# Kernel tuning notes

Measured on AMD Instinct MI355X. Metric: run time of the kernel, lower is better.

## Reference

```python
import jax, jax.numpy as jnp
import numpy as np

N_NODES = 100000
N_EDGES = 600000
IN_FEATS = 128
N_HIDDEN = 128
N_CLASSES = 64


def _glorot(key, shape):
    fan_in, fan_out = shape[1], shape[0]
    lim = np.sqrt(6.0 / (fan_in + fan_out)).astype(np.float32)
    return jax.random.uniform(key, shape, jnp.float32, -lim, lim)


def setup_inputs() -> dict:
    key = jax.random.key(0)
    ks = jax.random.split(key, 12)
    x = jax.random.normal(ks[0], (N_NODES, IN_FEATS), jnp.float32)
    edge_src = jax.random.randint(ks[1], (N_EDGES,), 0, N_NODES, jnp.int64 if jax.config.jax_enable_x64 else jnp.int32)
    edge_dst = jax.random.randint(ks[2], (N_EDGES,), 0, N_NODES, jnp.int64 if jax.config.jax_enable_x64 else jnp.int32)
    dims = [(IN_FEATS, N_HIDDEN), (N_HIDDEN, N_HIDDEN), (N_HIDDEN, N_CLASSES)]
    inp = {"x": x, "edge_src": edge_src, "edge_dst": edge_dst}
    for i, (din, dout) in enumerate(dims, start=1):
        inp[f"W_self{i}"] = _glorot(ks[2 + 3 * i], (dout, din))
        inp[f"W_neigh{i}"] = _glorot(ks[3 + 3 * i], (dout, din))
        inp[f"b{i}"] = jnp.zeros((dout,), jnp.float32)
    return inp


def _sage_conv(h, edge_src, edge_dst, W_self, W_neigh, b):
    # mean-aggregate neighbor features: gather at src, segment-mean at dst
    msgs = h[edge_src]                                   # [E, din] irregular gather
    agg = jax.ops.segment_sum(msgs, edge_dst, num_segments=h.shape[0])
    deg = jax.ops.segment_sum(jnp.ones_like(edge_dst, dtype=h.dtype), edge_dst,
                              num_segments=h.shape[0])
    h_neigh = agg / jnp.maximum(deg, 1.0)[:, None]
    # fc_self(h) + fc_neigh(h_neigh) + bias  (DGL SAGEConv 'mean')
    return h @ W_self.T + h_neigh @ W_neigh.T + b


def reference(x, edge_src, edge_dst,
              W_self1, W_neigh1, b1,
              W_self2, W_neigh2, b2,
              W_self3, W_neigh3, b3):
    h = _sage_conv(x, edge_src, edge_dst, W_self1, W_neigh1, b1)
    h = jax.nn.relu(h)  # dropout is identity at inference
    h = _sage_conv(h, edge_src, edge_dst, W_self2, W_neigh2, b2)
    h = jax.nn.relu(h)
    h = _sage_conv(h, edge_src, edge_dst, W_self3, W_neigh3, b3)
    return h
```

## Files before the change

kernel.cpp:

```cpp
#include <hip/hip_runtime.h>

#define NN 100000
#define NE 600000
#define FD 128
#define NB ((NN + 255) / 256)

typedef __attribute__((ext_vector_type(8))) short bf16x8;
typedef __attribute__((ext_vector_type(4))) float f32x4;

__device__ __forceinline__ unsigned short f2bf(float x) {
    unsigned int u = __float_as_uint(x);
    u += 0x7FFFu + ((u >> 16) & 1u);
    return (unsigned short)(u >> 16);
}

__global__ __launch_bounds__(256) void hist_kernel(const int* __restrict__ dst,
                                                   int* __restrict__ cnt, int E) {
    int e = blockIdx.x * 256 + threadIdx.x;
    if (e < E) atomicAdd(&cnt[dst[e]], 1);
}

__global__ __launch_bounds__(256) void scan_blocks(const int* __restrict__ cnt,
                                                   int* __restrict__ bsum) {
    __shared__ int s[256];
    int i = blockIdx.x * 256 + threadIdx.x;
    int t = threadIdx.x;
    s[t] = (i < NN) ? cnt[i] : 0;
    __syncthreads();
    for (int off = 128; off > 0; off >>= 1) {
        if (t < off) s[t] += s[t + off];
        __syncthreads();
    }
    if (t == 0) bsum[blockIdx.x] = s[0];
}

__global__ __launch_bounds__(512) void scan_top(int* __restrict__ bsum,
                                                int* __restrict__ row_ptr) {
    __shared__ int s[512];
    int t = threadIdx.x;
    int v = (t < NB) ? bsum[t] : 0;
    s[t] = v;
    __syncthreads();
    for (int off = 1; off < 512; off <<= 1) {
        int x = (t >= off) ? s[t - off] : 0;
        __syncthreads();
        s[t] += x;
        __syncthreads();
    }
    if (t < NB) bsum[t] = s[t] - v;
    if (t == 0) row_ptr[NN] = NE;
}

__global__ __launch_bounds__(256) void scan_write(const int* __restrict__ cnt,
                                                  const int* __restrict__ bofs,
                                                  int* __restrict__ row_ptr) {
    __shared__ int s[256];
    int i = blockIdx.x * 256 + threadIdx.x;
    int t = threadIdx.x;
    int v = (i < NN) ? cnt[i] : 0;
    s[t] = v;
    __syncthreads();
    for (int off = 1; off < 256; off <<= 1) {
        int x = (t >= off) ? s[t - off] : 0;
        __syncthreads();
        s[t] += x;
        __syncthreads();
    }
    if (i < NN) row_ptr[i] = s[t] - v + bofs[blockIdx.x];
}

__global__ __launch_bounds__(256) void fill_kernel(const int* __restrict__ src,
                                                   const int* __restrict__ dst,
                                                   int* __restrict__ cursor,
                                                   int* __restrict__ col, int E) {
    int e = blockIdx.x * 256 + threadIdx.x;
    if (e < E) {
        int p = atomicAdd(&cursor[dst[e]], 1);
        col[p] = src[e];
    }
}

__global__ __launch_bounds__(256) void cvt_kernel(const float* __restrict__ x,
                                                  unsigned short* __restrict__ xb,
                                                  int n4) {
    int i = blockIdx.x * 256 + threadIdx.x;
    if (i < n4) {
        float4 v = reinterpret_cast<const float4*>(x)[i];
        uint2 o;
        o.x = (unsigned)f2bf(v.x) | ((unsigned)f2bf(v.y) << 16);
        o.y = (unsigned)f2bf(v.z) | ((unsigned)f2bf(v.w) << 16);
        reinterpret_cast<uint2*>(xb)[i] = o;
    }
}

__global__ __launch_bounds__(256) void wcvt_kernel(const float* __restrict__ Ws,
                                                   const float* __restrict__ Wn,
                                                   unsigned short* __restrict__ Wb,
                                                   int rows) {
    int tid = blockIdx.x * 256 + threadIdx.x;
    if (tid >= rows * 64) return;
    int row = tid >> 6;
    int k   = (tid & 63) * 4;
    const float* src = (k < 128) ? (Ws + (size_t)row * 128 + k)
                                 : (Wn + (size_t)row * 128 + (k - 128));
    float4 v = *reinterpret_cast<const float4*>(src);
    uint2 o;
    o.x = (unsigned)f2bf(v.x) | ((unsigned)f2bf(v.y) << 16);
    o.y = (unsigned)f2bf(v.z) | ((unsigned)f2bf(v.w) << 16);
    *reinterpret_cast<uint2*>(Wb + (size_t)row * 256 + k) = o;
}

__device__ __forceinline__ void bf2_acc(unsigned v, float& ax, float& ay) {
    ax += __uint_as_float(v << 16);
    ay += __uint_as_float(v & 0xFFFF0000u);
}

__global__ __launch_bounds__(256) void agg_kernel(const unsigned short* __restrict__ h,
                                                  const int* __restrict__ rp,
                                                  const int* __restrict__ col,
                                                  unsigned short* __restrict__ agg) {
    int w    = (blockIdx.x * 256 + threadIdx.x) >> 6;
    int lane = threadIdx.x & 63;
    if (w >= NN) return;
    int beg = __builtin_amdgcn_readfirstlane(rp[w]);
    int end = __builtin_amdgcn_readfirstlane(rp[w + 1]);
    const unsigned short* hl = h + lane * 2;
    float ax = 0.f, ay = 0.f;
    int e = beg;
    for (; e + 4 <= end; e += 4) {
        int s0 = col[e + 0], s1 = col[e + 1], s2 = col[e + 2], s3 = col[e + 3];
        unsigned v0 = *reinterpret_cast<const unsigned*>(hl + (size_t)s0 * FD);
        unsigned v1 = *reinterpret_cast<const unsigned*>(hl + (size_t)s1 * FD);
        unsigned v2 = *reinterpret_cast<const unsigned*>(hl + (size_t)s2 * FD);
        unsigned v3 = *reinterpret_cast<const unsigned*>(hl + (size_t)s3 * FD);
        bf2_acc(v0, ax, ay);
        bf2_acc(v1, ax, ay);
        bf2_acc(v2, ax, ay);
        bf2_acc(v3, ax, ay);
    }
    if (e + 2 <= end) {
        int s0 = col[e + 0], s1 = col[e + 1];
        unsigned v0 = *reinterpret_cast<const unsigned*>(hl + (size_t)s0 * FD);
        unsigned v1 = *reinterpret_cast<const unsigned*>(hl + (size_t)s1 * FD);
        bf2_acc(v0, ax, ay);
        bf2_acc(v1, ax, ay);
        e += 2;
    }
    if (e < end) {
        int s0 = col[e];
        unsigned v0 = *reinterpret_cast<const unsigned*>(hl + (size_t)s0 * FD);
        bf2_acc(v0, ax, ay);
    }
    float inv = 1.0f / fmaxf((float)(end - beg), 1.0f);
    ax *= inv;
    ay *= inv;
    *reinterpret_cast<unsigned*>(agg + (size_t)w * FD + lane * 2) =
        (unsigned)f2bf(ax) | ((unsigned)f2bf(ay) << 16);
}

template <int BN, bool RELU, bool OUTBF16>
__global__ __launch_bounds__(256, 3) void mfma_gemm(const unsigned short* __restrict__ Ah,
                                                    const unsigned short* __restrict__ Ag,
                                                    const unsigned short* __restrict__ Wb,
                                                    const float* __restrict__ bias,
                                                    void* __restrict__ outp, int N) {
    __shared__ char lds[16384 + BN * 256];
    char* Al = lds;
    char* Bl = lds + 16384;

    const int t   = threadIdx.x;
    const int n0  = blockIdx.x * 64;
    const int w   = t >> 6;
    const int l   = t & 63;
    const int lo4 = l & 15;
    const int hi  = l >> 4;
    const int xr  = (lo4 & 7) << 4;

    f32x4 acc[BN / 16];
#pragma unroll
    for (int f = 0; f < BN / 16; ++f) acc[f] = {0.f, 0.f, 0.f, 0.f};

#pragma unroll
    for (int kc = 0; kc < 2; ++kc) {
        const unsigned short* Asrc = kc ? Ag : Ah;
#pragma unroll
        for (int p = 0; p < 4; ++p) {
            int c   = t + p * 256;
            int row = c >> 4;
            int ch  = c & 15;
            int n   = n0 + row;
            uint4 v = make_uint4(0u, 0u, 0u, 0u);
            if (n < N) v = *reinterpret_cast<const uint4*>(Asrc + (size_t)n * FD + ch * 8);
            *reinterpret_cast<uint4*>(Al + ((row * 256 + ch * 16) ^ ((row & 7) << 4))) = v;
        }
#pragma unroll
        for (int p = 0; p < BN / 16; ++p) {
            int c   = t + p * 256;
            int row = c >> 4;
            int ch  = c & 15;
            uint4 v = *reinterpret_cast<const uint4*>(Wb + (size_t)row * 256 + kc * 128 + ch * 8);
            *reinterpret_cast<uint4*>(Bl + ((row * 256 + ch * 16) ^ ((row & 7) << 4))) = v;
        }
        __syncthreads();

        const char* Arow = Al + (w * 16 + lo4) * 256;
#pragma unroll
        for (int ks = 0; ks < 4; ++ks) {
            int koff = (ks * 64 + hi * 16) ^ xr;
            bf16x8 a = *reinterpret_cast<const bf16x8*>(Arow + koff);
#pragma unroll
            for (int f = 0; f < BN / 16; ++f) {
                bf16x8 b = *reinterpret_cast<const bf16x8*>(Bl + (f * 16 + lo4) * 256 + koff);
                acc[f] = __builtin_amdgcn_mfma_f32_16x16x32_bf16(a, b, acc[f], 0, 0, 0);
            }
        }
        __syncthreads();
    }

    unsigned short* hout = (unsigned short*)outp;
    float* fout = (float*)outp;
    const int rbase = n0 + w * 16 + hi * 4;
#pragma unroll
    for (int f = 0; f < BN / 16; ++f) {
        int col  = f * 16 + lo4;
        float bv = bias[col];
#pragma unroll
        for (int r = 0; r < 4; ++r) {
            int n = rbase + r;
            if (n < N) {
                float v = acc[f][r] + bv;
                if (RELU) v = fmaxf(v, 0.f);
                if (OUTBF16) hout[(size_t)n * 128 + col] = f2bf(v);
                else         fout[(size_t)n * BN + col] = v;
            }
        }
    }
}

extern "C" void kernel_launch(void* const* d_in, const int* in_sizes, int n_in,
                              void* d_out, int out_size, void* d_ws, size_t ws_size,
                              hipStream_t stream) {
    const float* x        = (const float*)d_in[0];
    const int*   edge_src = (const int*)d_in[1];
    const int*   edge_dst = (const int*)d_in[2];
    const float* Ws1 = (const float*)d_in[3];
    const float* Wn1 = (const float*)d_in[4];
    const float* b1  = (const float*)d_in[5];
    const float* Ws2 = (const float*)d_in[6];
    const float* Wn2 = (const float*)d_in[7];
    const float* b2  = (const float*)d_in[8];
    const float* Ws3 = (const float*)d_in[9];
    const float* Wn3 = (const float*)d_in[10];
    const float* b3  = (const float*)d_in[11];
    float* out = (float*)d_out;

    unsigned short* x_bf = (unsigned short*)d_ws;
    unsigned short* h_a  = x_bf + (size_t)NN * FD;
    unsigned short* h_b  = h_a + (size_t)NN * FD;
    unsigned short* aggb = h_b + (size_t)NN * FD;
    int* cursor = (int*)(aggb + (size_t)NN * FD);
    int* bsum   = (int*)aggb;
    int* col_src = (int*)d_out;
    int* row_ptr = col_src + NE;
    unsigned short* wb1 = (unsigned short*)(col_src + NE + NN + 4);
    unsigned short* wb2 = wb1 + 128 * 256;
    unsigned short* wb3 = (unsigned short*)cursor;

    const int edgeGrid = (NE + 255) / 256;
    const int aggGrid  = NN / 4;
    const int rowGrid  = (NN + 63) / 64;

    cvt_kernel<<<(NN * FD / 4 + 255) / 256, 256, 0, stream>>>(x, x_bf, NN * FD / 4);
    wcvt_kernel<<<32, 256, 0, stream>>>(Ws1, Wn1, wb1, 128);
    wcvt_kernel<<<32, 256, 0, stream>>>(Ws2, Wn2, wb2, 128);

    hipMemsetAsync(cursor, 0, (size_t)NN * sizeof(int), stream);
    hist_kernel<<<edgeGrid, 256, 0, stream>>>(edge_dst, cursor, NE);
    scan_blocks<<<NB, 256, 0, stream>>>(cursor, bsum);
    scan_top<<<1, 512, 0, stream>>>(bsum, row_ptr);
    scan_write<<<NB, 256, 0, stream>>>(cursor, bsum, row_ptr);
    hipMemcpyAsync(cursor, row_ptr, (size_t)NN * sizeof(int),
                   hipMemcpyDeviceToDevice, stream);
    fill_kernel<<<edgeGrid, 256, 0, stream>>>(edge_src, edge_dst, cursor,
                                              col_src, NE);
    wcvt_kernel<<<16, 256, 0, stream>>>(Ws3, Wn3, wb3, 64);

    agg_kernel<<<aggGrid, 256, 0, stream>>>(x_bf, row_ptr, col_src, aggb);
    mfma_gemm<128, true, true><<<rowGrid, 256, 0, stream>>>(
        x_bf, aggb, wb1, b1, h_a, NN);

    agg_kernel<<<aggGrid, 256, 0, stream>>>(h_a, row_ptr, col_src, aggb);
    mfma_gemm<128, true, true><<<rowGrid, 256, 0, stream>>>(
        h_a, aggb, wb2, b2, h_b, NN);

    agg_kernel<<<aggGrid, 256, 0, stream>>>(h_b, row_ptr, col_src, aggb);
    mfma_gemm<64, false, false><<<rowGrid, 256, 0, stream>>>(
        h_b, aggb, wb3, b3, out, NN);
}
```

Measured before the change: 359.6 us.

## Make GEMM persistent with resident weights and double-buffered A tiles; unroll gather by 8

```diff
diff --git a/kernel.cpp b/kernel.cpp
--- a/kernel.cpp
+++ b/kernel.cpp
@@ -4,6 +4,7 @@
 #define NE 600000
 #define FD 128
 #define NB ((NN + 255) / 256)
+#define NTILES ((NN + 63) / 64)
 
 typedef __attribute__((ext_vector_type(8))) short bf16x8;
 typedef __attribute__((ext_vector_type(4))) float f32x4;
@@ -126,30 +127,18 @@
     int end = __builtin_amdgcn_readfirstlane(rp[w + 1]);
     const unsigned short* hl = h + lane * 2;
     float ax = 0.f, ay = 0.f;
-    int e = beg;
-    for (; e + 4 <= end; e += 4) {
-        int s0 = col[e + 0], s1 = col[e + 1], s2 = col[e + 2], s3 = col[e + 3];
-        unsigned v0 = *reinterpret_cast<const unsigned*>(hl + (size_t)s0 * FD);
-        unsigned v1 = *reinterpret_cast<const unsigned*>(hl + (size_t)s1 * FD);
-        unsigned v2 = *reinterpret_cast<const unsigned*>(hl + (size_t)s2 * FD);
-        unsigned v3 = *reinterpret_cast<const unsigned*>(hl + (size_t)s3 * FD);
-        bf2_acc(v0, ax, ay);
-        bf2_acc(v1, ax, ay);
-        bf2_acc(v2, ax, ay);
-        bf2_acc(v3, ax, ay);
-    }
-    if (e + 2 <= end) {
-        int s0 = col[e + 0], s1 = col[e + 1];
-        unsigned v0 = *reinterpret_cast<const unsigned*>(hl + (size_t)s0 * FD);
-        unsigned v1 = *reinterpret_cast<const unsigned*>(hl + (size_t)s1 * FD);
-        bf2_acc(v0, ax, ay);
-        bf2_acc(v1, ax, ay);
-        e += 2;
-    }
-    if (e < end) {
-        int s0 = col[e];
-        unsigned v0 = *reinterpret_cast<const unsigned*>(hl + (size_t)s0 * FD);
-        bf2_acc(v0, ax, ay);
+    if (beg < end) {
+        int last = end - 1;
+        for (int e = beg; e < end; e += 8) {
+#pragma unroll
+            for (int i = 0; i < 8; ++i) {
+                int ee  = e + i;
+                int idx = col[ee <= last ? ee : last];
+                unsigned v = *reinterpret_cast<const unsigned*>(hl + (size_t)idx * FD);
+                if (ee > last) v = 0u;
+                bf2_acc(v, ax, ay);
+            }
+        }
     }
     float inv = 1.0f / fmaxf((float)(end - beg), 1.0f);
     ax *= inv;
@@ -158,80 +147,120 @@
         (unsigned)f2bf(ax) | ((unsigned)f2bf(ay) << 16);
 }
 
-template <int BN, bool RELU, bool OUTBF16>
-__global__ __launch_bounds__(256, 3) void mfma_gemm(const unsigned short* __restrict__ Ah,
+template <int CT, bool RELU, bool OUTBF16, int OSTRIDE>
+__global__ __launch_bounds__(256, 2) void mfma_gemm(const unsigned short* __restrict__ Ah,
                                                     const unsigned short* __restrict__ Ag,
                                                     const unsigned short* __restrict__ Wb,
                                                     const float* __restrict__ bias,
                                                     void* __restrict__ outp, int N) {
-    __shared__ char lds[16384 + BN * 256];
-    char* Al = lds;
-    char* Bl = lds + 16384;
-
-    const int t   = threadIdx.x;
-    const int n0  = blockIdx.x * 64;
+    __shared__ char lds[65536];
+    char* Bl = lds + 32768;
+
+    const int t       = threadIdx.x;
+    const int bid     = blockIdx.x;
+    const int colhalf = (CT == 2) ? (bid & 1) : 0;
+    const int tstart  = (CT == 2) ? (bid >> 1) : bid;
+    const int tstride = gridDim.x / CT;
+    const int jbase   = colhalf * 64;
+
     const int w   = t >> 6;
     const int l   = t & 63;
     const int lo4 = l & 15;
     const int hi  = l >> 4;
     const int xr  = (lo4 & 7) << 4;
 
-    f32x4 acc[BN / 16];
-#pragma unroll
-    for (int f = 0; f < BN / 16; ++f) acc[f] = {0.f, 0.f, 0.f, 0.f};
-
-#pragma unroll
-    for (int kc = 0; kc < 2; ++kc) {
-        const unsigned short* Asrc = kc ? Ag : Ah;
+    {
+        uint4 r[8];
+#pragma unroll
+        for (int p = 0; p < 8; ++p) {
+            int c = t + p * 256;
+            int row = c >> 5, ch = c & 31;
+            r[p] = *reinterpret_cast<const uint4*>(
+                Wb + (size_t)(jbase + row) * 256 + ch * 8);
+        }
+#pragma unroll
+        for (int p = 0; p < 8; ++p) {
+            int c = t + p * 256;
+            int row = c >> 5, ch = c & 31;
+            *reinterpret_cast<uint4*>(
+                Bl + ((row * 512 + ch * 16) ^ ((row & 7) << 4))) = r[p];
+        }
+    }
+
+    uint4 ar[4];
+    auto A_LOAD = [&](int tl, int kc) {
+        const unsigned short* As = kc ? Ag : Ah;
 #pragma unroll
         for (int p = 0; p < 4; ++p) {
-            int c   = t + p * 256;
-            int row = c >> 4;
-            int ch  = c & 15;
-            int n   = n0 + row;
-            uint4 v = make_uint4(0u, 0u, 0u, 0u);
-            if (n < N) v = *reinterpret_cast<const uint4*>(Asrc + (size_t)n * FD + ch * 8);
-            *reinterpret_cast<uint4*>(Al + ((row * 256 + ch * 16) ^ ((row & 7) << 4))) = v;
-        }
-#pragma unroll
-        for (int p = 0; p < BN / 16; ++p) {
-            int c   = t + p * 256;
-            int row = c >> 4;
-            int ch  = c & 15;
-            uint4 v = *reinterpret_cast<const uint4*>(Wb + (size_t)row * 256 + kc * 128 + ch * 8);
-            *reinterpret_cast<uint4*>(Bl + ((row * 256 + ch * 16) ^ ((row & 7) << 4))) = v;
-        }
-        __syncthreads();
-
-        const char* Arow = Al + (w * 16 + lo4) * 256;
-#pragma unroll
-        for (int ks = 0; ks < 4; ++ks) {
-            int koff = (ks * 64 + hi * 16) ^ xr;
-            bf16x8 a = *reinterpret_cast<const bf16x8*>(Arow + koff);
-#pragma unroll
-            for (int f = 0; f < BN / 16; ++f) {
-                bf16x8 b = *reinterpret_cast<const bf16x8*>(Bl + (f * 16 + lo4) * 256 + koff);
-                acc[f] = __builtin_amdgcn_mfma_f32_16x16x32_bf16(a, b, acc[f], 0, 0, 0);
-            }
-        }
-        __syncthreads();
-    }
+            int c = t + p * 256;
+            int row = c >> 4, ch = c & 15;
+            int n = tl * 64 + row;
+            if (n >= N) n = N - 1;
+            ar[p] = *reinterpret_cast<const uint4*>(As + (size_t)n * FD + ch * 8);
+        }
+    };
+    auto A_WRITE = [&](int buf) {
+        char* Ab = lds + buf * 16384;
+#pragma unroll
+        for (int p = 0; p < 4; ++p) {
+            int c = t + p * 256;
+            int row = c >> 4, ch = c & 15;
+            *reinterpret_cast<uint4*>(
+                Ab + ((row * 256 + ch * 16) ^ ((row & 7) << 4))) = ar[p];
+        }
+    };
+
+    f32x4 acc[4];
+#pragma unroll
+    for (int f = 0; f < 4; ++f) acc[f] = {0.f, 0.f, 0.f, 0.f};
+
+    const int mytiles = (NTILES - 1 - tstart) / tstride + 1;
+    const int total   = mytiles * 2;
 
     unsigned short* hout = (unsigned short*)outp;
     float* fout = (float*)outp;
-    const int rbase = n0 + w * 16 + hi * 4;
-#pragma unroll
-    for (int f = 0; f < BN / 16; ++f) {
-        int col  = f * 16 + lo4;
-        float bv = bias[col];
-#pragma unroll
-        for (int r = 0; r < 4; ++r) {
-            int n = rbase + r;
-            if (n < N) {
-                float v = acc[f][r] + bv;
-                if (RELU) v = fmaxf(v, 0.f);
-                if (OUTBF16) hout[(size_t)n * 128 + col] = f2bf(v);
-                else         fout[(size_t)n * BN + col] = v;
+
+    A_LOAD(tstart, 0);
+    for (int i = 0; i < total; ++i) {
+        const int b  = i & 1;
+        const int kc = i & 1;
+        A_WRITE(b);
+        __syncthreads();
+        if (i + 1 < total) {
+            int ni = i + 1;
+            A_LOAD(tstart + (ni >> 1) * tstride, ni & 1);
+        }
+        const char* Arow = lds + b * 16384 + (w * 16 + lo4) * 256;
+#pragma unroll
+        for (int ks = 0; ks < 4; ++ks) {
+            int akoff = (ks * 64 + hi * 16) ^ xr;
+            bf16x8 a = *reinterpret_cast<const bf16x8*>(Arow + akoff);
+#pragma unroll
+            for (int f = 0; f < 4; ++f) {
+                int brow = f * 16 + lo4;
+                int bk   = (kc * 256 + ks * 64 + hi * 16) ^ ((brow & 7) << 4);
+                bf16x8 bb = *reinterpret_cast<const bf16x8*>(Bl + brow * 512 + bk);
+                acc[f] = __builtin_amdgcn_mfma_f32_16x16x32_bf16(a, bb, acc[f], 0, 0, 0);
+            }
+        }
+        if (kc == 1) {
+            int tl    = tstart + (i >> 1) * tstride;
+            int rbase = tl * 64 + w * 16 + hi * 4;
+#pragma unroll
+            for (int f = 0; f < 4; ++f) {
+                int col  = jbase + f * 16 + lo4;
+                float bv = bias[col];
+#pragma unroll
+                for (int r = 0; r < 4; ++r) {
+                    int n = rbase + r;
+                    if (n < N) {
+                        float v = acc[f][r] + bv;
+                        if (RELU) v = fmaxf(v, 0.f);
+                        if (OUTBF16) hout[(size_t)n * OSTRIDE + col] = f2bf(v);
+                        else         fout[(size_t)n * OSTRIDE + col] = v;
+                    }
+                }
+                acc[f] = {0.f, 0.f, 0.f, 0.f};
             }
         }
     }
@@ -268,7 +297,6 @@
 
     const int edgeGrid = (NE + 255) / 256;
     const int aggGrid  = NN / 4;
-    const int rowGrid  = (NN + 63) / 64;
 
     cvt_kernel<<<(NN * FD / 4 + 255) / 256, 256, 0, stream>>>(x, x_bf, NN * FD / 4);
     wcvt_kernel<<<32, 256, 0, stream>>>(Ws1, Wn1, wb1, 128);
@@ -286,14 +314,14 @@
     wcvt_kernel<<<16, 256, 0, stream>>>(Ws3, Wn3, wb3, 64);
 
     agg_kernel<<<aggGrid, 256, 0, stream>>>(x_bf, row_ptr, col_src, aggb);
-    mfma_gemm<128, true, true><<<rowGrid, 256, 0, stream>>>(
+    mfma_gemm<2, true, true, 128><<<512, 256, 0, stream>>>(
         x_bf, aggb, wb1, b1, h_a, NN);
 
     agg_kernel<<<aggGrid, 256, 0, stream>>>(h_a, row_ptr, col_src, aggb);
-    mfma_gemm<128, true, true><<<rowGrid, 256, 0, stream>>>(
+    mfma_gemm<2, true, true, 128><<<512, 256, 0, stream>>>(
         h_a, aggb, wb2, b2, h_b, NN);
 
     agg_kernel<<<aggGrid, 256, 0, stream>>>(h_b, row_ptr, col_src, aggb);
-    mfma_gemm<64, false, false><<<rowGrid, 256, 0, stream>>>(
+    mfma_gemm<1, false, false, 64><<<512, 256, 0, stream>>>(
         h_b, aggb, wb3, b3, out, NN);
 }
```

Result: slower. 445.2 us (+23.8%).

## Hold weights in registers with persistent grid-stride MFMA GEMM tiles

Applied to the files above, without the earlier changes.

```diff
diff --git a/kernel.cpp b/kernel.cpp
--- a/kernel.cpp
+++ b/kernel.cpp
@@ -158,80 +158,69 @@
         (unsigned)f2bf(ax) | ((unsigned)f2bf(ay) << 16);
 }
 
-template <int BN, bool RELU, bool OUTBF16>
-__global__ __launch_bounds__(256, 3) void mfma_gemm(const unsigned short* __restrict__ Ah,
-                                                    const unsigned short* __restrict__ Ag,
-                                                    const unsigned short* __restrict__ Wb,
-                                                    const float* __restrict__ bias,
-                                                    void* __restrict__ outp, int N) {
-    __shared__ char lds[16384 + BN * 256];
-    char* Al = lds;
-    char* Bl = lds + 16384;
+template <int NWC, bool RELU, bool OUTBF16, int OSTRIDE>
+__global__ __launch_bounds__(256) void mfma_gemm(const unsigned short* __restrict__ Ah,
+                                                 const unsigned short* __restrict__ Ag,
+                                                 const unsigned short* __restrict__ Wb,
+                                                 const float* __restrict__ bias,
+                                                 void* __restrict__ outp) {
+    constexpr int TR   = (4 / NWC) * 16;
+    constexpr int NTIL = NN / TR;
 
     const int t   = threadIdx.x;
-    const int n0  = blockIdx.x * 64;
     const int w   = t >> 6;
     const int l   = t & 63;
     const int lo4 = l & 15;
     const int hi  = l >> 4;
-    const int xr  = (lo4 & 7) << 4;
-
-    f32x4 acc[BN / 16];
-#pragma unroll
-    for (int f = 0; f < BN / 16; ++f) acc[f] = {0.f, 0.f, 0.f, 0.f};
-
-#pragma unroll
-    for (int kc = 0; kc < 2; ++kc) {
-        const unsigned short* Asrc = kc ? Ag : Ah;
-#pragma unroll
-        for (int p = 0; p < 4; ++p) {
-            int c   = t + p * 256;
-            int row = c >> 4;
-            int ch  = c & 15;
-            int n   = n0 + row;
-            uint4 v = make_uint4(0u, 0u, 0u, 0u);
-            if (n < N) v = *reinterpret_cast<const uint4*>(Asrc + (size_t)n * FD + ch * 8);
-            *reinterpret_cast<uint4*>(Al + ((row * 256 + ch * 16) ^ ((row & 7) << 4))) = v;
-        }
-#pragma unroll
-        for (int p = 0; p < BN / 16; ++p) {
-            int c   = t + p * 256;
-            int row = c >> 4;
-            int ch  = c & 15;
-            uint4 v = *reinterpret_cast<const uint4*>(Wb + (size_t)row * 256 + kc * 128 + ch * 8);
-            *reinterpret_cast<uint4*>(Bl + ((row * 256 + ch * 16) ^ ((row & 7) << 4))) = v;
-        }
-        __syncthreads();
-
-        const char* Arow = Al + (w * 16 + lo4) * 256;
-#pragma unroll
-        for (int ks = 0; ks < 4; ++ks) {
-            int koff = (ks * 64 + hi * 16) ^ xr;
-            bf16x8 a = *reinterpret_cast<const bf16x8*>(Arow + koff);
-#pragma unroll
-            for (int f = 0; f < BN / 16; ++f) {
-                bf16x8 b = *reinterpret_cast<const bf16x8*>(Bl + (f * 16 + lo4) * 256 + koff);
-                acc[f] = __builtin_amdgcn_mfma_f32_16x16x32_bf16(a, b, acc[f], 0, 0, 0);
-            }
-        }
-        __syncthreads();
-    }
+    const int jw      = (w % NWC) * 32;
+    const int row_off = (w / NWC) * 16;
+
+    bf16x8 breg[2][8];
+#pragma unroll
+    for (int f = 0; f < 2; ++f)
+#pragma unroll
+        for (int ks = 0; ks < 8; ++ks)
+            breg[f][ks] = *reinterpret_cast<const bf16x8*>(
+                Wb + (size_t)(jw + f * 16 + lo4) * 256 + ks * 32 + hi * 8);
 
     unsigned short* hout = (unsigned short*)outp;
     float* fout = (float*)outp;
-    const int rbase = n0 + w * 16 + hi * 4;
-#pragma unroll
-    for (int f = 0; f < BN / 16; ++f) {
-        int col  = f * 16 + lo4;
-        float bv = bias[col];
+    const float bv0 = bias[jw + lo4];
+    const float bv1 = bias[jw + 16 + lo4];
+
+    for (int tile = blockIdx.x; tile < NTIL; tile += gridDim.x) {
+        const int row = tile * TR + row_off + lo4;
+        const unsigned short* Ar = Ah + (size_t)row * FD;
+        const unsigned short* Gr = Ag + (size_t)row * FD;
+        bf16x8 a[8];
+#pragma unroll
+        for (int ks = 0; ks < 4; ++ks)
+            a[ks] = *reinterpret_cast<const bf16x8*>(Ar + ks * 32 + hi * 8);
+#pragma unroll
+        for (int ks = 0; ks < 4; ++ks)
+            a[4 + ks] = *reinterpret_cast<const bf16x8*>(Gr + ks * 32 + hi * 8);
+
+        f32x4 acc0 = {0.f, 0.f, 0.f, 0.f};
+        f32x4 acc1 = {0.f, 0.f, 0.f, 0.f};
+#pragma unroll
+        for (int ks = 0; ks < 8; ++ks) {
+            acc0 = __builtin_amdgcn_mfma_f32_16x16x32_bf16(a[ks], breg[0][ks], acc0, 0, 0, 0);
+            acc1 = __builtin_amdgcn_mfma_f32_16x16x32_bf16(a[ks], breg[1][ks], acc1, 0, 0, 0);
+        }
+
+        const int rbase = tile * TR + row_off + hi * 4;
 #pragma unroll
         for (int r = 0; r < 4; ++r) {
-            int n = rbase + r;
-            if (n < N) {
-                float v = acc[f][r] + bv;
-                if (RELU) v = fmaxf(v, 0.f);
-                if (OUTBF16) hout[(size_t)n * 128 + col] = f2bf(v);
-                else         fout[(size_t)n * BN + col] = v;
+            float v0 = acc0[r] + bv0;
+            float v1 = acc1[r] + bv1;
+            if (RELU) { v0 = fmaxf(v0, 0.f); v1 = fmaxf(v1, 0.f); }
+            const size_t n = (size_t)(rbase + r);
+            if (OUTBF16) {
+                hout[n * OSTRIDE + jw + lo4]      = f2bf(v0);
+                hout[n * OSTRIDE + jw + 16 + lo4] = f2bf(v1);
+            } else {
+                fout[n * OSTRIDE + jw + lo4]      = v0;
+                fout[n * OSTRIDE + jw + 16 + lo4] = v1;
             }
         }
     }
@@ -268,7 +257,6 @@
 
     const int edgeGrid = (NE + 255) / 256;
     const int aggGrid  = NN / 4;
-    const int rowGrid  = (NN + 63) / 64;
 
     cvt_kernel<<<(NN * FD / 4 + 255) / 256, 256, 0, stream>>>(x, x_bf, NN * FD / 4);
     wcvt_kernel<<<32, 256, 0, stream>>>(Ws1, Wn1, wb1, 128);
@@ -286,14 +274,14 @@
     wcvt_kernel<<<16, 256, 0, stream>>>(Ws3, Wn3, wb3, 64);
 
     agg_kernel<<<aggGrid, 256, 0, stream>>>(x_bf, row_ptr, col_src, aggb);
-    mfma_gemm<128, true, true><<<rowGrid, 256, 0, stream>>>(
-        x_bf, aggb, wb1, b1, h_a, NN);
+    mfma_gemm<4, true, true, 128><<<1024, 256, 0, stream>>>(
+        x_bf, aggb, wb1, b1, h_a);
 
     agg_kernel<<<aggGrid, 256, 0, stream>>>(h_a, row_ptr, col_src, aggb);
-    mfma_gemm<128, true, true><<<rowGrid, 256, 0, stream>>>(
-        h_a, aggb, wb2, b2, h_b, NN);
+    mfma_gemm<4, true, true, 128><<<1024, 256, 0, stream>>>(
+        h_a, aggb, wb2, b2, h_b);
 
     agg_kernel<<<aggGrid, 256, 0, stream>>>(h_b, row_ptr, col_src, aggb);
-    mfma_gemm<64, false, false><<<rowGrid, 256, 0, stream>>>(
-        h_b, aggb, wb3, b3, out, NN);
-}
+    mfma_gemm<2, false, false, 64><<<1024, 256, 0, stream>>>(
+        h_b, aggb, wb3, b3, out);
+}
```

Measured after the change: 366.0 us. Within noise of the previous version (+1.8%).
